# Kernel tuning notes

Hardware: AMD Instinct MI355X
Metric: run time of the kernel (lower is better)

The kernel has to match this reference:

```python
import jax, jax.numpy as jnp
from jax import lax
import numpy as np

HIDDEN = 40
NUM_LAYERS = 7
B, H, W = 16, 64, 64
KS = 7
PAD = KS // 2  # 3

# mask for conv_2d type 'A': zero rows below center, zero right-of-center in
# the center row, and zero the center tap itself
_m = np.ones((1, 1, KS, KS), np.float32)
_m[:, :, PAD + 1:, :] = 0
_m[:, :, PAD, PAD + 1:] = 0
_m[:, :, PAD, PAD] = 0
MASK_A = jnp.asarray(_m)


def conv2d(x, w, pad):
    return lax.conv_general_dilated(x, w, (1, 1), pad,
                                    dimension_numbers=('NCHW', 'OIHW', 'NCHW'))


def setup_inputs() -> dict:
    key = jax.random.key(0)
    ks = jax.random.split(key, 12)
    s = 0.05
    return {
        'input_tensor': jax.random.normal(ks[0], (B, 1, H, W), jnp.float32),
        'target_tensor': jax.random.normal(ks[1], (B, 1, H, W), jnp.float32),
        # masked conv_2d(7,1,80) applied to target
        'w_is': jax.random.normal(ks[2], (2 * HIDDEN, 1, KS, KS), jnp.float32) * s,
        'b_is': jnp.ones((2 * HIDDEN,), jnp.float32),
        # conv_i_s: Conv2d(1, 80, 7, pad 3)
        'w_cis': jax.random.normal(ks[3], (2 * HIDDEN, 1, KS, KS), jnp.float32) * s,
        'b_cis': jax.random.normal(ks[4], (2 * HIDDEN,), jnp.float32) * s,
        # row convs: Conv2d(40, 40, [1,3], pad [0,1])
        'w_rh': jax.random.normal(ks[5], (HIDDEN, HIDDEN, 1, 3), jnp.float32) * s,
        'b_rh': jax.random.normal(ks[6], (HIDDEN,), jnp.float32) * s,
        'w_rc': jax.random.normal(ks[7], (HIDDEN, HIDDEN, 1, 3), jnp.float32) * s,
        'b_rc': jax.random.normal(ks[8], (HIDDEN,), jnp.float32) * s,
        # per-layer cell 1x1 convs: 40 -> 160, stacked over layers
        'w_cell': jax.random.normal(ks[9], (NUM_LAYERS, 4 * HIDDEN, HIDDEN), jnp.float32) * s,
        'b_cell': jax.random.normal(ks[10], (NUM_LAYERS, 4 * HIDDEN), jnp.float32) * s,
        # conv_out: Conv2d(40, 256, 1)
        'w_out': jax.random.normal(ks[11], (256, HIDDEN), jnp.float32) * s,
        'b_out': jnp.zeros((256,), jnp.float32),
    }


def reference(input_tensor, target_tensor, w_is, b_is, w_cis, b_cis,
              w_rh, b_rh, w_rc, b_rc, w_cell, b_cell, w_out, b_out):
    same7 = ((PAD, PAD), (PAD, PAD))
    # i_s = cat([conv_i_s(input), masked_conv(target)], dim=1) -> [B, 160, H, W]
    i_s_input = conv2d(input_tensor, w_cis, same7) + b_cis[None, :, None, None]
    i_s_target = conv2d(target_tensor, w_is * MASK_A, same7) + b_is[None, :, None, None]
    i_s = jnp.concatenate([i_s_input, i_s_target], axis=1)

    h0 = jnp.zeros((B, HIDDEN, 1, W), i_s.dtype)
    c0 = jnp.zeros((B, HIDDEN, 1, W), i_s.dtype)

    def step(carry, x_t):  # x_t: [B, 160, 1, W]
        h, c = carry
        h = conv2d(h, w_rh, ((0, 0), (1, 1))) + b_rh[None, :, None, None]
        c = conv2d(c, w_rc, ((0, 0), (1, 1))) + b_rc[None, :, None, None]
        for l in range(NUM_LAYERS):
            h_conv = jnp.einsum('oc,bcrw->borw', w_cell[l], h) + b_cell[l][None, :, None, None]
            combined = x_t + h_conv
            cc_i, cc_f, cc_o, cc_g = jnp.split(combined, 4, axis=1)
            i = jax.nn.sigmoid(cc_i)
            f = jax.nn.sigmoid(cc_f)
            o = jax.nn.sigmoid(cc_o)
            g = jnp.tanh(cc_g)
            c = f * c + i * g
            h = o * jnp.tanh(c)
        return (h, c), h

    xs = jnp.moveaxis(i_s, 2, 0)[:, :, :, None, :]  # [H, B, 160, 1, W]
    _, hs = lax.scan(step, (h0, c0), xs)            # hs: [H, B, 40, 1, W]
    hidden = jnp.moveaxis(hs[:, :, :, 0, :], 0, 2)  # [B, 40, H, W]
    out = jnp.einsum('oc,bchw->bohw', w_out, hidden) + b_out[None, :, None, None]
    return jax.nn.relu(out)
```

## Files before the change

kernel.cpp:

```cpp
#include <hip/hip_runtime.h>


typedef __bf16 bf16x8 __attribute__((ext_vector_type(8)));
typedef __bf16 bf16x4 __attribute__((ext_vector_type(4)));
typedef float  f32x4  __attribute__((ext_vector_type(4)));

#define SC1 (-1.44269504089f)
#define SC2 (-2.88539008178f)

#define STP 56
#define HLS 896
#define CWS 17

#define BARRIER_LGKM() __asm__ volatile("s_waitcnt lgkmcnt(0)\ns_barrier" ::: "memory")

__global__ __launch_bounds__(256) void prep_kernel(
        const float* __restrict__ wcell, const float* __restrict__ wrh,
        const float* __restrict__ wrc, const float* __restrict__ bcell,
        const float* __restrict__ brh, const float* __restrict__ brc,
        __bf16* __restrict__ wsA) {
    int i = blockIdx.x * 256 + threadIdx.x;
    if (i >= 120832) return;
    float val = 0.0f;
    if (i < 35840) {
        int j = i & 7, lane = (i >> 3) & 63, lm = i >> 9;
        int mt = lm % 10, l = lm / 10;
        int k = (lane >> 4) * 8 + j, m = lane & 15, r = m & 3;
        int row = r * 40 + 4 * mt + (m >> 2);
        val = wcell[(l * 160 + row) * 40 + k] * (r == 3 ? SC2 : SC1);
    } else if (i < 71680) {
        int i2 = i - 35840;
        int j = i2 & 7, lane = (i2 >> 3) & 63, lm = i2 >> 9;
        int mt = lm % 10, l = lm / 10;
        int k = 32 + (lane >> 4) * 8 + j, m = lane & 15, r = m & 3;
        int row = r * 40 + 4 * mt + (m >> 2);
        float s = (r == 3 ? SC2 : SC1);
        if (k < 40)       val = wcell[(l * 160 + row) * 40 + k] * s;
        else if (k == 40) val = bcell[l * 160 + row] * s;
    } else if (i < 80896) {
        int i3 = i - 71680;
        int j = i3 & 7, lane = (i3 >> 3) & 63, idx = i3 >> 9;
        int mtc = idx % 3, t2 = idx / 3, dx = t2 % 3, cv = t2 / 3;
        int k = (lane >> 4) * 8 + j;
        int ch = 16 * mtc + (lane & 15);
        const float* w = cv ? wrc : wrh;
        if (ch < 40) val = w[(ch * 40 + k) * 3 + dx];
    } else if (i < 90112) {
        int i4 = i - 80896;
        int j = i4 & 7, lane = (i4 >> 3) & 63, idx = i4 >> 9;
        int mtc = idx % 3, t2 = idx / 3, dx = t2 % 3, cv = t2 / 3;
        int k = 32 + (lane >> 4) * 8 + j;
        int ch = 16 * mtc + (lane & 15);
        if (ch < 40) {
            const float* w = cv ? wrc : wrh;
            if (k < 40)                    val = w[(ch * 40 + k) * 3 + dx];
            else if (k == 40 && dx == 1)   val = (cv ? brc : brh)[ch];
        }
    } else if (i < 105472) {
        int i5 = i - 90112;
        int j = i5 & 7, lane = (i5 >> 3) & 63, idx = i5 >> 9;
        int mt = idx % 10, dx = idx / 10;
        int k = (lane >> 4) * 8 + j, m = lane & 15, r = m & 3;
        int row = r * 40 + 4 * mt + (m >> 2);
        float s = (r == 3 ? SC2 : SC1);
        float acc = 0.0f;
        for (int mm = 0; mm < 40; mm++)
            acc = __builtin_fmaf(wcell[row * 40 + mm],
                                 wrh[(mm * 40 + k) * 3 + dx], acc);
        val = acc * s;
    } else {
        int i6 = i - 105472;
        int j = i6 & 7, lane = (i6 >> 3) & 63, idx = i6 >> 9;
        int mt = idx % 10, dx = idx / 10;
        int k = 32 + (lane >> 4) * 8 + j, m = lane & 15, r = m & 3;
        int row = r * 40 + 4 * mt + (m >> 2);
        float s = (r == 3 ? SC2 : SC1);
        if (k < 40) {
            float acc = 0.0f;
            for (int mm = 0; mm < 40; mm++)
                acc = __builtin_fmaf(wcell[row * 40 + mm],
                                     wrh[(mm * 40 + k) * 3 + dx], acc);
            val = acc * s;
        } else if (k == 40 && dx == 1) {
            float acc = bcell[row];
            for (int mm = 0; mm < 40; mm++)
                acc = __builtin_fmaf(wcell[row * 40 + mm], brh[mm], acc);
            val = acc * s;
        }
    }
    wsA[i] = (__bf16)val;
}

__global__ __launch_bounds__(256) void conv7_kernel(
        const float* __restrict__ inp, const float* __restrict__ tgt,
        const float* __restrict__ w_is, const float* __restrict__ b_is,
        const float* __restrict__ w_cis, const float* __restrict__ b_cis,
        float* __restrict__ x_ws) {
    int b = blockIdx.x >> 6, y = blockIdx.x & 63;
    int tid = threadIdx.x, qq = tid >> 6, w = tid & 63;
    const float* ib = inp + b * 4096;
    const float* tb = tgt + b * 4096;
    float pin[7][7], ptg[4][7];
#pragma unroll
    for (int dy = 0; dy < 7; dy++) {
        int yy = y + dy - 3;
#pragma unroll
        for (int dx = 0; dx < 7; dx++) {
            int xx = w + dx - 3;
            bool ok = (yy >= 0 && yy < 64 && xx >= 0 && xx < 64);
            pin[dy][dx] = ok ? ib[yy * 64 + xx] : 0.0f;
            if (dy < 4) ptg[dy][dx] = ok ? tb[yy * 64 + xx] : 0.0f;
        }
    }
    int g = w >> 4, l16 = w & 15;
    for (int j = 0; j < 10; j++) {
        int cc = 4 * j + qq;
        int ccu = __builtin_amdgcn_readfirstlane(cc);
        float a0 = b_cis[ccu], a1 = b_cis[40 + ccu];
        float a2 = b_is[ccu], a3 = b_is[40 + ccu];
        const float* w0 = w_cis + ccu * 49;
        const float* w1 = w_cis + (40 + ccu) * 49;
        const float* w2 = w_is + ccu * 49;
        const float* w3 = w_is + (40 + ccu) * 49;
#pragma unroll
        for (int dy = 0; dy < 7; dy++)
#pragma unroll
            for (int dx = 0; dx < 7; dx++) {
                a0 = __builtin_fmaf(w0[dy * 7 + dx], pin[dy][dx], a0);
                a1 = __builtin_fmaf(w1[dy * 7 + dx], pin[dy][dx], a1);
            }
#pragma unroll
        for (int dy = 0; dy < 3; dy++)
#pragma unroll
            for (int dx = 0; dx < 7; dx++) {
                a2 = __builtin_fmaf(w2[dy * 7 + dx], ptg[dy][dx], a2);
                a3 = __builtin_fmaf(w3[dy * 7 + dx], ptg[dy][dx], a3);
            }
#pragma unroll
        for (int dx = 0; dx < 3; dx++) {
            a2 = __builtin_fmaf(w2[21 + dx], ptg[3][dx], a2);
            a3 = __builtin_fmaf(w3[21 + dx], ptg[3][dx], a3);
        }
        size_t idx = (size_t)((((b * 64 + y) * 4 + g) * 10 + j) * 4 + qq) * 64
                     + l16 * 4;
        *(f32x4*)&x_ws[idx] = f32x4{a0 * SC1, a1 * SC1, a2 * SC1, a3 * SC2};
    }
}

__global__ __launch_bounds__(640, 1) void rnn_kernel(
        const float* __restrict__ x_ws, const __bf16* __restrict__ wsA,
        float* __restrict__ hid_ws,
        unsigned long long* __restrict__ halo_ws) {
    __shared__ __align__(16) __bf16 hC[18 * STP + 64];
    __shared__ __align__(16) __bf16 cC[18 * STP + 64];
    __shared__ __align__(16) __bf16 hL[2 * HLS + 32];
    __shared__ float cwf[40 * CWS];
    __shared__ unsigned cflag[4];

    const int bid = blockIdx.x, g = bid >> 4, b = bid & 15;
    const int tid = threadIdx.x, wv = tid >> 6, lane = tid & 63;
    const int q = lane >> 4, l16 = lane & 15, cc = 4 * wv + q;
    const int W0 = g * 16;

    for (int i = tid; i < 536; i += 640) {
        ((float*)hC)[i] = 0.0f;
        ((float*)cC)[i] = 0.0f;
    }
    for (int i = tid; i < 912; i += 640)
        ((float*)hL)[i] = 0.0f;
    for (int i = tid; i < 40 * CWS; i += 640) cwf[i] = 0.0f;
    if (tid < 4) cflag[tid] = 0xFFFFFFFFu;
    __syncthreads();
    if (tid < 18) { hC[tid * STP + 40] = (__bf16)1.0f; cC[tid * STP + 40] = (__bf16)1.0f; }
    if (tid < 32) hL[(tid >> 4) * HLS + (tid & 15) * STP + 40] = (__bf16)1.0f;
    __syncthreads();

    bf16x8 a0c[6], a1c[6];
#pragma unroll
    for (int l = 1; l < 7; l++) {
        a0c[l - 1] = *(const bf16x8*)&wsA[((l * 10 + wv) * 64 + lane) * 8];
        a1c[l - 1] = *(const bf16x8*)&wsA[35840 + ((l * 10 + wv) * 64 + lane) * 8];
    }
    bf16x8 f0c[3], f1c[3];
#pragma unroll
    for (int dx = 0; dx < 3; dx++) {
        f0c[dx] = *(const bf16x8*)&wsA[90112 + ((dx * 10 + wv) * 64 + lane) * 8];
        f1c[dx] = *(const bf16x8*)&wsA[105472 + ((dx * 10 + wv) * 64 + lane) * 8];
    }
    bf16x8 cva0[3], cva1[3];
    if (wv >= 3 && wv < 6) {
        int mtc = wv - 3;
#pragma unroll
        for (int dx = 0; dx < 3; dx++) {
            int it = (3 + dx) * 3 + mtc;
            cva0[dx] = *(const bf16x8*)&wsA[71680 + (it * 64 + lane) * 8];
            cva1[dx] = *(const bf16x8*)&wsA[80896 + (it * 64 + lane) * 8];
        }
    }

    float c_reg = 0.0f;
    const size_t xstride = 10240;
    const size_t xbase0 = (size_t)(b * 64) * xstride
        + (((size_t)g * 10 + wv) * 4 + q) * 64 + l16 * 4;
    f32x4 xv = *(const f32x4*)&x_ws[xbase0];

    for (int t = 0; t < 64; t++) {
        f32x4 xn = xv;
        if (t < 63) xn = *(const f32x4*)&x_ws[xbase0 + (size_t)(t + 1) * xstride];

        if (wv >= 3 && wv < 6) {
            f32x4 ac = f32x4{0.f, 0.f, 0.f, 0.f};
#pragma unroll
            for (int dx = 0; dx < 3; dx++) {
                bf16x8 b0 = *(const bf16x8*)&cC[(l16 + dx) * STP + q * 8];
                bf16x8 b1 = *(const bf16x8*)&cC[(l16 + dx) * STP + 32 + q * 8];
                ac = __builtin_amdgcn_mfma_f32_16x16x32_bf16(cva0[dx], b0, ac, 0, 0, 0);
                ac = __builtin_amdgcn_mfma_f32_16x16x32_bf16(cva1[dx], b1, ac, 0, 0, 0);
            }
            int mtc = wv - 3, ch0 = 16 * mtc + 4 * q;
            if (ch0 < 40) {
#pragma unroll
                for (int r = 0; r < 4; r++) cwf[(ch0 + r) * CWS + l16] = ac[r];
            }
            __asm__ volatile("s_waitcnt lgkmcnt(0)" ::: "memory");
            if (lane == 0)
                __hip_atomic_store(&cflag[mtc], (unsigned)t,
                                   __ATOMIC_RELAXED, __HIP_MEMORY_SCOPE_WORKGROUP);
        }

        f32x4 acc0 = f32x4{0.f, 0.f, 0.f, 0.f};
#pragma unroll
        for (int dx = 0; dx < 3; dx++) {
            bf16x8 b0 = *(const bf16x8*)&hC[(l16 + dx) * STP + q * 8];
            bf16x8 b1 = *(const bf16x8*)&hC[(l16 + dx) * STP + 32 + q * 8];
            acc0 = __builtin_amdgcn_mfma_f32_16x16x32_bf16(f0c[dx], b0, acc0, 0, 0, 0);
            acc0 = __builtin_amdgcn_mfma_f32_16x16x32_bf16(f1c[dx], b1, acc0, 0, 0, 0);
        }
        {
            int jj = wv >> 2;
            while (__hip_atomic_load(&cflag[jj], __ATOMIC_RELAXED,
                                     __HIP_MEMORY_SCOPE_WORKGROUP) != (unsigned)t)
                __builtin_amdgcn_s_sleep(1);
            __asm__ volatile("" ::: "memory");
        }

#pragma unroll
        for (int l = 0; l < 7; l++) {
            f32x4 acc;
            if (l == 0) {
                acc = acc0;
                c_reg = cwf[cc * CWS + l16];
            } else {
                const __bf16* hb = &hL[(l & 1) * HLS];
                bf16x8 b0 = *(const bf16x8*)&hb[l16 * STP + q * 8];
                bf16x8 b1 = *(const bf16x8*)&hb[l16 * STP + 32 + q * 8];
                acc = __builtin_amdgcn_mfma_f32_16x16x32_bf16(
                    a0c[l - 1], b0, f32x4{0.f, 0.f, 0.f, 0.f}, 0, 0, 0);
                acc = __builtin_amdgcn_mfma_f32_16x16x32_bf16(a1c[l - 1], b1, acc, 0, 0, 0);
            }
            float Ei = __builtin_amdgcn_exp2f(fminf(acc[0] + xv[0], 44.f));
            float Ef = __builtin_amdgcn_exp2f(fminf(acc[1] + xv[1], 44.f));
            float Eo = __builtin_amdgcn_exp2f(fminf(acc[2] + xv[2], 44.f));
            float Eg = __builtin_amdgcn_exp2f(fminf(acc[3] + xv[3], 44.f));
            float f = __builtin_amdgcn_rcpf(1.0f + Ef);
            float ig = (1.0f - Eg) * __builtin_amdgcn_rcpf((1.0f + Ei) * (1.0f + Eg));
            float c = __builtin_fmaf(f, c_reg, ig);
            c_reg = c;
            float Ec = __builtin_amdgcn_exp2f(fminf(SC2 * c, 44.f));
            float h = (1.0f - Ec) * __builtin_amdgcn_rcpf((1.0f + Eo) * (1.0f + Ec));
            if (l < 6) {
                hL[((l + 1) & 1) * HLS + l16 * STP + cc] = (__bf16)h;
                BARRIER_LGKM();
            } else {
                hC[(l16 + 1) * STP + cc] = (__bf16)h;
                cC[(l16 + 1) * STP + cc] = (__bf16)c;
                hid_ws[(size_t)((b * 64 + t) * 40 + cc) * 64 + W0 + l16] = h;
                if (t < 63) {
                    unsigned short h16 = __builtin_bit_cast(unsigned short, (__bf16)h);
                    unsigned short c16 = __builtin_bit_cast(unsigned short, (__bf16)c);
                    unsigned long long v = ((unsigned long long)(unsigned)t << 32)
                        | ((unsigned)c16 << 16) | (unsigned)h16;
                    if (l16 == 0 && g > 0)
                        __hip_atomic_store(
                            &halo_ws[((bid * 2 + 0) * 2 + (t & 1)) * 40 + cc], v,
                            __ATOMIC_RELAXED, __HIP_MEMORY_SCOPE_AGENT);
                    if (l16 == 15 && g < 3)
                        __hip_atomic_store(
                            &halo_ws[((bid * 2 + 1) * 2 + (t & 1)) * 40 + cc], v,
                            __ATOMIC_RELAXED, __HIP_MEMORY_SCOPE_AGENT);
                }
            }
        }

        if (t < 63) {
            if (wv == 8 && g > 0 && lane < 40) {
                const unsigned long long* src =
                    &halo_ws[(((bid - 16) * 2 + 1) * 2 + (t & 1)) * 40 + lane];
                unsigned long long v = __hip_atomic_load(
                    src, __ATOMIC_RELAXED, __HIP_MEMORY_SCOPE_AGENT);
                while ((unsigned)(v >> 32) != (unsigned)t) {
                    __builtin_amdgcn_s_sleep(1);
                    v = __hip_atomic_load(src, __ATOMIC_RELAXED,
                                          __HIP_MEMORY_SCOPE_AGENT);
                }
                hC[lane] = __builtin_bit_cast(__bf16, (unsigned short)(v & 0xffffu));
                cC[lane] = __builtin_bit_cast(__bf16, (unsigned short)((v >> 16) & 0xffffu));
            }
            if (wv == 9 && g < 3 && lane < 40) {
                const unsigned long long* src =
                    &halo_ws[(((bid + 16) * 2 + 0) * 2 + (t & 1)) * 40 + lane];
                unsigned long long v = __hip_atomic_load(
                    src, __ATOMIC_RELAXED, __HIP_MEMORY_SCOPE_AGENT);
                while ((unsigned)(v >> 32) != (unsigned)t) {
                    __builtin_amdgcn_s_sleep(1);
                    v = __hip_atomic_load(src, __ATOMIC_RELAXED,
                                          __HIP_MEMORY_SCOPE_AGENT);
                }
                hC[17 * STP + lane] = __builtin_bit_cast(__bf16, (unsigned short)(v & 0xffffu));
                cC[17 * STP + lane] = __builtin_bit_cast(__bf16, (unsigned short)((v >> 16) & 0xffffu));
            }
        }
        BARRIER_LGKM();
        xv = xn;
    }
}

__global__ __launch_bounds__(256) void out_kernel(
        const float* __restrict__ hid_ws, const float* __restrict__ w_out,
        const float* __restrict__ b_out, float* __restrict__ out) {
    __shared__ float wlds[40 * 264];
    __shared__ float hlds[40 * 64];
    int b = blockIdx.x >> 6, y = blockIdx.x & 63;
    int tid = threadIdx.x;
    for (int i = tid; i < 10240; i += 256) {
        int o = i / 40, k = i - o * 40;
        wlds[k * 264 + o] = w_out[i];
    }
    const float* hbp = hid_ws + (size_t)(b * 64 + y) * 40 * 64;
    for (int i = tid; i < 2560; i += 256) hlds[i] = hbp[i];
    __syncthreads();

    int tn = tid & 7, tm = tid >> 3;
    int wbase = tn * 8, obase = tm * 8;
    float acc[8][8];
#pragma unroll
    for (int io = 0; io < 8; io++)
#pragma unroll
        for (int iw = 0; iw < 8; iw++) acc[io][iw] = 0.0f;

    for (int k = 0; k < 40; k++) {
        f32x4 hA = *(const f32x4*)&hlds[k * 64 + wbase];
        f32x4 hB = *(const f32x4*)&hlds[k * 64 + wbase + 4];
        f32x4 wA = *(const f32x4*)&wlds[k * 264 + obase];
        f32x4 wB = *(const f32x4*)&wlds[k * 264 + obase + 4];
#pragma unroll
        for (int io = 0; io < 8; io++) {
            float wo = (io < 4) ? wA[io] : wB[io - 4];
#pragma unroll
            for (int iw = 0; iw < 8; iw++) {
                float hx = (iw < 4) ? hA[iw] : hB[iw - 4];
                acc[io][iw] = __builtin_fmaf(wo, hx, acc[io][iw]);
            }
        }
    }
#pragma unroll
    for (int io = 0; io < 8; io++) {
        int o = obase + io;
        float bo = b_out[o];
        f32x4 s0, s1;
#pragma unroll
        for (int iw = 0; iw < 4; iw++)
            s0[iw] = fmaxf(acc[io][iw] + bo, 0.0f);
#pragma unroll
        for (int iw = 0; iw < 4; iw++)
            s1[iw] = fmaxf(acc[io][iw + 4] + bo, 0.0f);
        float* ob = out + (size_t)((b * 256 + o) * 64 + y) * 64 + wbase;
        *(f32x4*)ob = s0;
        *(f32x4*)(ob + 4) = s1;
    }
}

extern "C" void kernel_launch(void* const* d_in, const int* in_sizes, int n_in,
                              void* d_out, int out_size, void* d_ws,
                              size_t ws_size, hipStream_t stream) {
    const float* input  = (const float*)d_in[0];
    const float* target = (const float*)d_in[1];
    const float* w_is   = (const float*)d_in[2];
    const float* b_is   = (const float*)d_in[3];
    const float* w_cis  = (const float*)d_in[4];
    const float* b_cis  = (const float*)d_in[5];
    const float* w_rh   = (const float*)d_in[6];
    const float* b_rh   = (const float*)d_in[7];
    const float* w_rc   = (const float*)d_in[8];
    const float* b_rc   = (const float*)d_in[9];
    const float* w_cell = (const float*)d_in[10];
    const float* b_cell = (const float*)d_in[11];
    const float* w_out  = (const float*)d_in[12];
    const float* b_out  = (const float*)d_in[13];
    float* out = (float*)d_out;

    char* ws = (char*)d_ws;
    float*              x_ws    = (float*)ws;
    float*              hid_ws  = (float*)(ws + 41943040);
    __bf16*             wsA     = (__bf16*)(ws + 52428800);
    unsigned long long* halo_ws = (unsigned long long*)(ws + 52670464);

    prep_kernel<<<472, 256, 0, stream>>>(w_cell, w_rh, w_rc, b_cell, b_rh,
                                         b_rc, wsA);
    conv7_kernel<<<1024, 256, 0, stream>>>(input, target, w_is, b_is, w_cis,
                                           b_cis, x_ws);
    rnn_kernel<<<64, 640, 0, stream>>>(x_ws, wsA, hid_ws, halo_ws);
    out_kernel<<<1024, 256, 0, stream>>>(hid_ws, w_out, b_out, out);
}
```

Baseline: 369.4 us.

## Give each RNN wave two gate tiles and shrink the block to eight waves

The recurrent kernel moves from 10 waves, each owning one 16-row gate tile, to 5 compute waves that each own two tiles, plus 3 waves that handle the c-conv and halo exchange. The B operand loaded from LDS is shared by both tiles, so fewer waves take part in each of the per-layer barriers and fewer LDS reads are issued. In exchange, each compute wave runs a longer serial chain on the critical path and holds twice as many weight registers, which raises register pressure.

Result: slower. 395.8 us (+7.1%).

```diff
diff --git a/kernel.cpp b/kernel.cpp
--- a/kernel.cpp
+++ b/kernel.cpp
@@ -147,7 +147,7 @@
     }
 }
 
-__global__ __launch_bounds__(640, 1) void rnn_kernel(
+__global__ __launch_bounds__(512, 1) void rnn_kernel(
         const float* __restrict__ x_ws, const __bf16* __restrict__ wsA,
         float* __restrict__ hid_ws,
         unsigned long long* __restrict__ halo_ws) {
@@ -159,37 +159,46 @@
 
     const int bid = blockIdx.x, g = bid >> 4, b = bid & 15;
     const int tid = threadIdx.x, wv = tid >> 6, lane = tid & 63;
-    const int q = lane >> 4, l16 = lane & 15, cc = 4 * wv + q;
+    const int q = lane >> 4, l16 = lane & 15;
+    const int cc0 = 8 * wv + q;
     const int W0 = g * 16;
 
-    for (int i = tid; i < 536; i += 640) {
+    for (int i = tid; i < 536; i += 512) {
         ((float*)hC)[i] = 0.0f;
         ((float*)cC)[i] = 0.0f;
     }
-    for (int i = tid; i < 912; i += 640)
+    for (int i = tid; i < 912; i += 512)
         ((float*)hL)[i] = 0.0f;
-    for (int i = tid; i < 40 * CWS; i += 640) cwf[i] = 0.0f;
+    for (int i = tid; i < 40 * CWS; i += 512) cwf[i] = 0.0f;
     if (tid < 4) cflag[tid] = 0xFFFFFFFFu;
     __syncthreads();
     if (tid < 18) { hC[tid * STP + 40] = (__bf16)1.0f; cC[tid * STP + 40] = (__bf16)1.0f; }
     if (tid < 32) hL[(tid >> 4) * HLS + (tid & 15) * STP + 40] = (__bf16)1.0f;
     __syncthreads();
 
-    bf16x8 a0c[6], a1c[6];
-#pragma unroll
-    for (int l = 1; l < 7; l++) {
-        a0c[l - 1] = *(const bf16x8*)&wsA[((l * 10 + wv) * 64 + lane) * 8];
-        a1c[l - 1] = *(const bf16x8*)&wsA[35840 + ((l * 10 + wv) * 64 + lane) * 8];
-    }
-    bf16x8 f0c[3], f1c[3];
-#pragma unroll
-    for (int dx = 0; dx < 3; dx++) {
-        f0c[dx] = *(const bf16x8*)&wsA[90112 + ((dx * 10 + wv) * 64 + lane) * 8];
-        f1c[dx] = *(const bf16x8*)&wsA[105472 + ((dx * 10 + wv) * 64 + lane) * 8];
+    bf16x8 a0c[6][2], a1c[6][2];
+    bf16x8 f0c[3][2], f1c[3][2];
+    if (wv < 5) {
+#pragma unroll
+        for (int l = 1; l < 7; l++)
+#pragma unroll
+            for (int tt = 0; tt < 2; tt++) {
+                int mt = 2 * wv + tt;
+                a0c[l - 1][tt] = *(const bf16x8*)&wsA[((l * 10 + mt) * 64 + lane) * 8];
+                a1c[l - 1][tt] = *(const bf16x8*)&wsA[35840 + ((l * 10 + mt) * 64 + lane) * 8];
+            }
+#pragma unroll
+        for (int dx = 0; dx < 3; dx++)
+#pragma unroll
+            for (int tt = 0; tt < 2; tt++) {
+                int mt = 2 * wv + tt;
+                f0c[dx][tt] = *(const bf16x8*)&wsA[90112 + ((dx * 10 + mt) * 64 + lane) * 8];
+                f1c[dx][tt] = *(const bf16x8*)&wsA[105472 + ((dx * 10 + mt) * 64 + lane) * 8];
+            }
     }
     bf16x8 cva0[3], cva1[3];
-    if (wv >= 3 && wv < 6) {
-        int mtc = wv - 3;
+    if (wv >= 5) {
+        int mtc = wv - 5;
 #pragma unroll
         for (int dx = 0; dx < 3; dx++) {
             int it = (3 + dx) * 3 + mtc;
@@ -198,17 +207,25 @@
         }
     }
 
-    float c_reg = 0.0f;
     const size_t xstride = 10240;
-    const size_t xbase0 = (size_t)(b * 64) * xstride
-        + (((size_t)g * 10 + wv) * 4 + q) * 64 + l16 * 4;
-    f32x4 xv = *(const f32x4*)&x_ws[xbase0];
+    size_t xb[2];
+    {
+        int mt0 = (wv < 5) ? 2 * wv : 0, mt1 = (wv < 5) ? 2 * wv + 1 : 0;
+        xb[0] = (size_t)(b * 64) * xstride + (((size_t)g * 10 + mt0) * 4 + q) * 64 + l16 * 4;
+        xb[1] = (size_t)(b * 64) * xstride + (((size_t)g * 10 + mt1) * 4 + q) * 64 + l16 * 4;
+    }
+    f32x4 xv[2], xn[2];
+    xv[0] = *(const f32x4*)&x_ws[xb[0]];
+    xv[1] = *(const f32x4*)&x_ws[xb[1]];
 
     for (int t = 0; t < 64; t++) {
-        f32x4 xn = xv;
-        if (t < 63) xn = *(const f32x4*)&x_ws[xbase0 + (size_t)(t + 1) * xstride];
-
-        if (wv >= 3 && wv < 6) {
+        xn[0] = xv[0]; xn[1] = xv[1];
+        if (wv < 5 && t < 63) {
+            xn[0] = *(const f32x4*)&x_ws[xb[0] + (size_t)(t + 1) * xstride];
+            xn[1] = *(const f32x4*)&x_ws[xb[1] + (size_t)(t + 1) * xstride];
+        }
+
+        if (wv >= 5) {
             f32x4 ac = f32x4{0.f, 0.f, 0.f, 0.f};
 #pragma unroll
             for (int dx = 0; dx < 3; dx++) {
@@ -217,7 +234,7 @@
                 ac = __builtin_amdgcn_mfma_f32_16x16x32_bf16(cva0[dx], b0, ac, 0, 0, 0);
                 ac = __builtin_amdgcn_mfma_f32_16x16x32_bf16(cva1[dx], b1, ac, 0, 0, 0);
             }
-            int mtc = wv - 3, ch0 = 16 * mtc + 4 * q;
+            int mtc = wv - 5, ch0 = 16 * mtc + 4 * q;
             if (ch0 < 40) {
 #pragma unroll
                 for (int r = 0; r < 4; r++) cwf[(ch0 + r) * CWS + l16] = ac[r];
@@ -228,72 +245,89 @@
                                    __ATOMIC_RELAXED, __HIP_MEMORY_SCOPE_WORKGROUP);
         }
 
-        f32x4 acc0 = f32x4{0.f, 0.f, 0.f, 0.f};
-#pragma unroll
-        for (int dx = 0; dx < 3; dx++) {
-            bf16x8 b0 = *(const bf16x8*)&hC[(l16 + dx) * STP + q * 8];
-            bf16x8 b1 = *(const bf16x8*)&hC[(l16 + dx) * STP + 32 + q * 8];
-            acc0 = __builtin_amdgcn_mfma_f32_16x16x32_bf16(f0c[dx], b0, acc0, 0, 0, 0);
-            acc0 = __builtin_amdgcn_mfma_f32_16x16x32_bf16(f1c[dx], b1, acc0, 0, 0, 0);
-        }
-        {
-            int jj = wv >> 2;
+        f32x4 acc0[2];
+        if (wv < 5) {
+            acc0[0] = f32x4{0.f, 0.f, 0.f, 0.f};
+            acc0[1] = f32x4{0.f, 0.f, 0.f, 0.f};
+#pragma unroll
+            for (int dx = 0; dx < 3; dx++) {
+                bf16x8 b0 = *(const bf16x8*)&hC[(l16 + dx) * STP + q * 8];
+                bf16x8 b1 = *(const bf16x8*)&hC[(l16 + dx) * STP + 32 + q * 8];
+#pragma unroll
+                for (int tt = 0; tt < 2; tt++) {
+                    acc0[tt] = __builtin_amdgcn_mfma_f32_16x16x32_bf16(f0c[dx][tt], b0, acc0[tt], 0, 0, 0);
+                    acc0[tt] = __builtin_amdgcn_mfma_f32_16x16x32_bf16(f1c[dx][tt], b1, acc0[tt], 0, 0, 0);
+                }
+            }
+            int jj = wv >> 1;
             while (__hip_atomic_load(&cflag[jj], __ATOMIC_RELAXED,
                                      __HIP_MEMORY_SCOPE_WORKGROUP) != (unsigned)t)
                 __builtin_amdgcn_s_sleep(1);
             __asm__ volatile("" ::: "memory");
         }
 
+        float crg[2];
 #pragma unroll
         for (int l = 0; l < 7; l++) {
-            f32x4 acc;
-            if (l == 0) {
-                acc = acc0;
-                c_reg = cwf[cc * CWS + l16];
-            } else {
-                const __bf16* hb = &hL[(l & 1) * HLS];
-                bf16x8 b0 = *(const bf16x8*)&hb[l16 * STP + q * 8];
-                bf16x8 b1 = *(const bf16x8*)&hb[l16 * STP + 32 + q * 8];
-                acc = __builtin_amdgcn_mfma_f32_16x16x32_bf16(
-                    a0c[l - 1], b0, f32x4{0.f, 0.f, 0.f, 0.f}, 0, 0, 0);
-                acc = __builtin_amdgcn_mfma_f32_16x16x32_bf16(a1c[l - 1], b1, acc, 0, 0, 0);
-            }
-            float Ei = __builtin_amdgcn_exp2f(fminf(acc[0] + xv[0], 44.f));
-            float Ef = __builtin_amdgcn_exp2f(fminf(acc[1] + xv[1], 44.f));
-            float Eo = __builtin_amdgcn_exp2f(fminf(acc[2] + xv[2], 44.f));
-            float Eg = __builtin_amdgcn_exp2f(fminf(acc[3] + xv[3], 44.f));
-            float f = __builtin_amdgcn_rcpf(1.0f + Ef);
-            float ig = (1.0f - Eg) * __builtin_amdgcn_rcpf((1.0f + Ei) * (1.0f + Eg));
-            float c = __builtin_fmaf(f, c_reg, ig);
-            c_reg = c;
-            float Ec = __builtin_amdgcn_exp2f(fminf(SC2 * c, 44.f));
-            float h = (1.0f - Ec) * __builtin_amdgcn_rcpf((1.0f + Eo) * (1.0f + Ec));
-            if (l < 6) {
-                hL[((l + 1) & 1) * HLS + l16 * STP + cc] = (__bf16)h;
-                BARRIER_LGKM();
-            } else {
-                hC[(l16 + 1) * STP + cc] = (__bf16)h;
-                cC[(l16 + 1) * STP + cc] = (__bf16)c;
-                hid_ws[(size_t)((b * 64 + t) * 40 + cc) * 64 + W0 + l16] = h;
-                if (t < 63) {
-                    unsigned short h16 = __builtin_bit_cast(unsigned short, (__bf16)h);
-                    unsigned short c16 = __builtin_bit_cast(unsigned short, (__bf16)c);
-                    unsigned long long v = ((unsigned long long)(unsigned)t << 32)
-                        | ((unsigned)c16 << 16) | (unsigned)h16;
-                    if (l16 == 0 && g > 0)
-                        __hip_atomic_store(
-                            &halo_ws[((bid * 2 + 0) * 2 + (t & 1)) * 40 + cc], v,
-                            __ATOMIC_RELAXED, __HIP_MEMORY_SCOPE_AGENT);
-                    if (l16 == 15 && g < 3)
-                        __hip_atomic_store(
-                            &halo_ws[((bid * 2 + 1) * 2 + (t & 1)) * 40 + cc], v,
-                            __ATOMIC_RELAXED, __HIP_MEMORY_SCOPE_AGENT);
+            if (wv < 5) {
+                f32x4 av[2];
+                if (l == 0) {
+                    av[0] = acc0[0]; av[1] = acc0[1];
+                    crg[0] = cwf[cc0 * CWS + l16];
+                    crg[1] = cwf[(cc0 + 4) * CWS + l16];
+                } else {
+                    const __bf16* hb = &hL[(l & 1) * HLS];
+                    bf16x8 b0 = *(const bf16x8*)&hb[l16 * STP + q * 8];
+                    bf16x8 b1 = *(const bf16x8*)&hb[l16 * STP + 32 + q * 8];
+#pragma unroll
+                    for (int tt = 0; tt < 2; tt++) {
+                        av[tt] = __builtin_amdgcn_mfma_f32_16x16x32_bf16(
+                            a0c[l - 1][tt], b0, f32x4{0.f, 0.f, 0.f, 0.f}, 0, 0, 0);
+                        av[tt] = __builtin_amdgcn_mfma_f32_16x16x32_bf16(
+                            a1c[l - 1][tt], b1, av[tt], 0, 0, 0);
+                    }
                 }
-            }
+#pragma unroll
+                for (int tt = 0; tt < 2; tt++) {
+                    int cc = cc0 + 4 * tt;
+                    float Ei = __builtin_amdgcn_exp2f(fminf(av[tt][0] + xv[tt][0], 44.f));
+                    float Ef = __builtin_amdgcn_exp2f(fminf(av[tt][1] + xv[tt][1], 44.f));
+                    float Eo = __builtin_amdgcn_exp2f(fminf(av[tt][2] + xv[tt][2], 44.f));
+                    float Eg = __builtin_amdgcn_exp2f(fminf(av[tt][3] + xv[tt][3], 44.f));
+                    float f = __builtin_amdgcn_rcpf(1.0f + Ef);
+                    float ig = (1.0f - Eg) * __builtin_amdgcn_rcpf((1.0f + Ei) * (1.0f + Eg));
+                    float c = __builtin_fmaf(f, crg[tt], ig);
+                    crg[tt] = c;
+                    float Ec = __builtin_amdgcn_exp2f(fminf(SC2 * c, 44.f));
+                    float h = (1.0f - Ec) * __builtin_amdgcn_rcpf((1.0f + Eo) * (1.0f + Ec));
+                    if (l < 6) {
+                        hL[((l + 1) & 1) * HLS + l16 * STP + cc] = (__bf16)h;
+                    } else {
+                        hC[(l16 + 1) * STP + cc] = (__bf16)h;
+                        cC[(l16 + 1) * STP + cc] = (__bf16)c;
+                        hid_ws[(size_t)((b * 64 + t) * 40 + cc) * 64 + W0 + l16] = h;
+                        if (t < 63) {
+                            unsigned short h16 = __builtin_bit_cast(unsigned short, (__bf16)h);
+                            unsigned short c16 = __builtin_bit_cast(unsigned short, (__bf16)c);
+                            unsigned long long v = ((unsigned long long)(unsigned)t << 32)
+                                | ((unsigned)c16 << 16) | (unsigned)h16;
+                            if (l16 == 0 && g > 0)
+                                __hip_atomic_store(
+                                    &halo_ws[((bid * 2 + 0) * 2 + (t & 1)) * 40 + cc], v,
+                                    __ATOMIC_RELAXED, __HIP_MEMORY_SCOPE_AGENT);
+                            if (l16 == 15 && g < 3)
+                                __hip_atomic_store(
+                                    &halo_ws[((bid * 2 + 1) * 2 + (t & 1)) * 40 + cc], v,
+                                    __ATOMIC_RELAXED, __HIP_MEMORY_SCOPE_AGENT);
+                        }
+                    }
+                }
+            }
+            if (l < 6) BARRIER_LGKM();
         }
 
         if (t < 63) {
-            if (wv == 8 && g > 0 && lane < 40) {
+            if (wv == 5 && g > 0 && lane < 40) {
                 const unsigned long long* src =
                     &halo_ws[(((bid - 16) * 2 + 1) * 2 + (t & 1)) * 40 + lane];
                 unsigned long long v = __hip_atomic_load(
@@ -306,7 +340,7 @@
                 hC[lane] = __builtin_bit_cast(__bf16, (unsigned short)(v & 0xffffu));
                 cC[lane] = __builtin_bit_cast(__bf16, (unsigned short)((v >> 16) & 0xffffu));
             }
-            if (wv == 9 && g < 3 && lane < 40) {
+            if (wv == 6 && g < 3 && lane < 40) {
                 const unsigned long long* src =
                     &halo_ws[(((bid + 16) * 2 + 0) * 2 + (t & 1)) * 40 + lane];
                 unsigned long long v = __hip_atomic_load(
@@ -321,7 +355,7 @@
             }
         }
         BARRIER_LGKM();
-        xv = xn;
+        xv[0] = xn[0]; xv[1] = xn[1];
     }
 }
 
@@ -409,6 +443,6 @@
                                          b_rc, wsA);
     conv7_kernel<<<1024, 256, 0, stream>>>(input, target, w_is, b_is, w_cis,
                                            b_cis, x_ws);
-    rnn_kernel<<<64, 640, 0, stream>>>(x_ws, wsA, hid_ws, halo_ws);
+    rnn_kernel<<<64, 512, 0, stream>>>(x_ws, wsA, hid_ws, halo_ws);
     out_kernel<<<1024, 256, 0, stream>>>(hid_ws, w_out, b_out, out);
 }
```

## Fuse conv7 into RNN kernel with worker blocks and an atomic completion counter

Applied to the files above, without the earlier changes.

Merges the 7x7 input convolution and the recurrent kernel into one launch. 176 extra worker blocks compute x_ws and bump a global atomic counter, while the 64 RNN blocks load their weights and spin on that counter before starting the scan. This saves one kernel launch and lets the RNN setup overlap the convolution. The cost is that all 240 blocks must be co-resident for the spin-wait to be safe, and the wait loop has a timeout that could let the RNN read incomplete data.

After: 458.4 us. 1.24x slower.

```diff
diff --git a/kernel.cpp b/kernel.cpp
--- a/kernel.cpp
+++ b/kernel.cpp
@@ -11,6 +11,7 @@
 #define STP 56
 #define HLS 896
 #define CWS 17
+#define NWRK 176u
 
 #define BARRIER_LGKM() __asm__ volatile("s_waitcnt lgkmcnt(0)\ns_barrier" ::: "memory")
 
@@ -18,9 +19,12 @@
         const float* __restrict__ wcell, const float* __restrict__ wrh,
         const float* __restrict__ wrc, const float* __restrict__ bcell,
         const float* __restrict__ brh, const float* __restrict__ brc,
-        __bf16* __restrict__ wsA) {
+        __bf16* __restrict__ wsA, unsigned* __restrict__ xcnt) {
     int i = blockIdx.x * 256 + threadIdx.x;
-    if (i >= 120832) return;
+    if (i >= 120832) {
+        if (i == 120832) xcnt[0] = 0u;
+        return;
+    }
     float val = 0.0f;
     if (i < 35840) {
         int j = i & 7, lane = (i >> 3) & 63, lm = i >> 9;
@@ -91,74 +95,86 @@
     wsA[i] = (__bf16)val;
 }
 
-__global__ __launch_bounds__(256) void conv7_kernel(
+__global__ __launch_bounds__(640, 1) void fused_kernel(
         const float* __restrict__ inp, const float* __restrict__ tgt,
         const float* __restrict__ w_is, const float* __restrict__ b_is,
         const float* __restrict__ w_cis, const float* __restrict__ b_cis,
-        float* __restrict__ x_ws) {
-    int b = blockIdx.x >> 6, y = blockIdx.x & 63;
-    int tid = threadIdx.x, qq = tid >> 6, w = tid & 63;
-    const float* ib = inp + b * 4096;
-    const float* tb = tgt + b * 4096;
-    float pin[7][7], ptg[4][7];
-#pragma unroll
-    for (int dy = 0; dy < 7; dy++) {
-        int yy = y + dy - 3;
-#pragma unroll
-        for (int dx = 0; dx < 7; dx++) {
-            int xx = w + dx - 3;
-            bool ok = (yy >= 0 && yy < 64 && xx >= 0 && xx < 64);
-            pin[dy][dx] = ok ? ib[yy * 64 + xx] : 0.0f;
-            if (dy < 4) ptg[dy][dx] = ok ? tb[yy * 64 + xx] : 0.0f;
-        }
-    }
-    int g = w >> 4, l16 = w & 15;
-    for (int j = 0; j < 10; j++) {
-        int cc = 4 * j + qq;
-        int ccu = __builtin_amdgcn_readfirstlane(cc);
-        float a0 = b_cis[ccu], a1 = b_cis[40 + ccu];
-        float a2 = b_is[ccu], a3 = b_is[40 + ccu];
-        const float* w0 = w_cis + ccu * 49;
-        const float* w1 = w_cis + (40 + ccu) * 49;
-        const float* w2 = w_is + ccu * 49;
-        const float* w3 = w_is + (40 + ccu) * 49;
-#pragma unroll
-        for (int dy = 0; dy < 7; dy++)
-#pragma unroll
-            for (int dx = 0; dx < 7; dx++) {
-                a0 = __builtin_fmaf(w0[dy * 7 + dx], pin[dy][dx], a0);
-                a1 = __builtin_fmaf(w1[dy * 7 + dx], pin[dy][dx], a1);
-            }
-#pragma unroll
-        for (int dy = 0; dy < 3; dy++)
-#pragma unroll
-            for (int dx = 0; dx < 7; dx++) {
-                a2 = __builtin_fmaf(w2[dy * 7 + dx], ptg[dy][dx], a2);
-                a3 = __builtin_fmaf(w3[dy * 7 + dx], ptg[dy][dx], a3);
-            }
-#pragma unroll
-        for (int dx = 0; dx < 3; dx++) {
-            a2 = __builtin_fmaf(w2[21 + dx], ptg[3][dx], a2);
-            a3 = __builtin_fmaf(w3[21 + dx], ptg[3][dx], a3);
-        }
-        size_t idx = (size_t)((((b * 64 + y) * 4 + g) * 10 + j) * 4 + qq) * 64
-                     + l16 * 4;
-        *(f32x4*)&x_ws[idx] = f32x4{a0 * SC1, a1 * SC1, a2 * SC1, a3 * SC2};
-    }
-}
-
-__global__ __launch_bounds__(640, 1) void rnn_kernel(
-        const float* __restrict__ x_ws, const __bf16* __restrict__ wsA,
-        float* __restrict__ hid_ws,
-        unsigned long long* __restrict__ halo_ws) {
-    __shared__ __align__(16) __bf16 hC[18 * STP + 64];
-    __shared__ __align__(16) __bf16 cC[18 * STP + 64];
-    __shared__ __align__(16) __bf16 hL[2 * HLS + 32];
-    __shared__ float cwf[40 * CWS];
+        float* __restrict__ x_ws, const __bf16* __restrict__ wsA,
+        float* __restrict__ hid_ws, unsigned long long* __restrict__ halo_ws,
+        unsigned* __restrict__ xcnt) {
+    __shared__ __align__(16) unsigned char smem[83968];
     __shared__ unsigned cflag[4];
-
-    const int bid = blockIdx.x, g = bid >> 4, b = bid & 15;
-    const int tid = threadIdx.x, wv = tid >> 6, lane = tid & 63;
+    const int bid = blockIdx.x;
+    const int tid = threadIdx.x;
+
+    if (bid >= 64) {
+        for (int p = bid - 64; p < 1024; p += 176) {
+            const int y = p >> 4, b = p & 15;
+            const int j = tid >> 6, w = tid & 63;
+            const float* ib = inp + b * 4096;
+            const float* tb = tgt + b * 4096;
+            float pin[7][7], ptg[4][7];
+#pragma unroll
+            for (int dy = 0; dy < 7; dy++) {
+                int yy = y + dy - 3;
+#pragma unroll
+                for (int dx = 0; dx < 7; dx++) {
+                    int xx = w + dx - 3;
+                    bool ok = (yy >= 0 && yy < 64 && xx >= 0 && xx < 64);
+                    pin[dy][dx] = ok ? ib[yy * 64 + xx] : 0.0f;
+                    if (dy < 4) ptg[dy][dx] = ok ? tb[yy * 64 + xx] : 0.0f;
+                }
+            }
+            int g = w >> 4, l16 = w & 15;
+#pragma unroll 1
+            for (int qq = 0; qq < 4; qq++) {
+                int cc = 4 * j + qq;
+                int ccu = __builtin_amdgcn_readfirstlane(cc);
+                float a0 = b_cis[ccu], a1 = b_cis[40 + ccu];
+                float a2 = b_is[ccu], a3 = b_is[40 + ccu];
+                const float* w0 = w_cis + ccu * 49;
+                const float* w1 = w_cis + (40 + ccu) * 49;
+                const float* w2 = w_is + ccu * 49;
+                const float* w3 = w_is + (40 + ccu) * 49;
+#pragma unroll
+                for (int dy = 0; dy < 7; dy++)
+#pragma unroll
+                    for (int dx = 0; dx < 7; dx++) {
+                        a0 = __builtin_fmaf(w0[dy * 7 + dx], pin[dy][dx], a0);
+                        a1 = __builtin_fmaf(w1[dy * 7 + dx], pin[dy][dx], a1);
+                    }
+#pragma unroll
+                for (int dy = 0; dy < 3; dy++)
+#pragma unroll
+                    for (int dx = 0; dx < 7; dx++) {
+                        a2 = __builtin_fmaf(w2[dy * 7 + dx], ptg[dy][dx], a2);
+                        a3 = __builtin_fmaf(w3[dy * 7 + dx], ptg[dy][dx], a3);
+                    }
+#pragma unroll
+                for (int dx = 0; dx < 3; dx++) {
+                    a2 = __builtin_fmaf(w2[21 + dx], ptg[3][dx], a2);
+                    a3 = __builtin_fmaf(w3[21 + dx], ptg[3][dx], a3);
+                }
+                size_t idx = (size_t)((((b * 64 + y) * 4 + g) * 10 + j) * 4 + qq) * 64
+                             + l16 * 4;
+                *(f32x4*)&x_ws[idx] = f32x4{a0 * SC1, a1 * SC1, a2 * SC1, a3 * SC2};
+            }
+        }
+        __threadfence();
+        __syncthreads();
+        if (tid == 0)
+            __hip_atomic_fetch_add(xcnt, 1u, __ATOMIC_RELEASE,
+                                   __HIP_MEMORY_SCOPE_AGENT);
+        return;
+    }
+
+    __bf16* hC  = (__bf16*)smem;
+    __bf16* cC  = (__bf16*)(smem + 4096);
+    __bf16* hL  = (__bf16*)(smem + 8192);
+    float*  cwf = (float*)(smem + 16384);
+
+    const int g = bid >> 4, b = bid & 15;
+    const int wv = tid >> 6, lane = tid & 63;
     const int q = lane >> 4, l16 = lane & 15, cc = 4 * wv + q;
     const int W0 = g * 16;
 
@@ -197,6 +213,16 @@
             cva1[dx] = *(const bf16x8*)&wsA[80896 + (it * 64 + lane) * 8];
         }
     }
+
+    if (tid == 0) {
+        int gk = 0;
+        while (__hip_atomic_load(xcnt, __ATOMIC_ACQUIRE,
+                                 __HIP_MEMORY_SCOPE_AGENT) < NWRK) {
+            if (++gk > (1 << 17)) break;
+            __builtin_amdgcn_s_sleep(8);
+        }
+    }
+    __syncthreads();
 
     float c_reg = 0.0f;
     const size_t xstride = 10240;
@@ -404,11 +430,12 @@
     float*              hid_ws  = (float*)(ws + 41943040);
     __bf16*             wsA     = (__bf16*)(ws + 52428800);
     unsigned long long* halo_ws = (unsigned long long*)(ws + 52670464);
-
-    prep_kernel<<<472, 256, 0, stream>>>(w_cell, w_rh, w_rc, b_cell, b_rh,
-                                         b_rc, wsA);
-    conv7_kernel<<<1024, 256, 0, stream>>>(input, target, w_is, b_is, w_cis,
-                                           b_cis, x_ws);
-    rnn_kernel<<<64, 640, 0, stream>>>(x_ws, wsA, hid_ws, halo_ws);
+    unsigned*           xcnt    = (unsigned*)(ws + 52752384);
+
+    prep_kernel<<<473, 256, 0, stream>>>(w_cell, w_rh, w_rc, b_cell, b_rh,
+                                         b_rc, wsA, xcnt);
+    fused_kernel<<<240, 640, 0, stream>>>(input, target, w_is, b_is, w_cis,
+                                          b_cis, x_ws, wsA, hid_ws, halo_ws,
+                                          xcnt);
     out_kernel<<<1024, 256, 0, stream>>>(hid_ws, w_out, b_out, out);
 }
```

## Fuse output 1x1 conv and ReLU into RNN kernel via bf16 MFMA

Applied to the files above, without the earlier changes.

Removes the separate out_kernel and the hidden-state workspace round trip. The RNN kernel now computes the 256-channel output projection for the previous row from the bf16 h tile in LDS using MFMA, with the bias folded in as an extra K element. Waves 0-7 do this work inside the serial timestep loop, and the last row is handled after the loop. This saves one launch and the global write and read of hidden, but adds MFMA work and many scattered global stores to the latency-critical recurrence, and the projection now uses bf16 instead of fp32.

New measurement: 366.6 us (median of 2 runs). About the same (-0.8%).

```diff
diff --git a/kernel.cpp b/kernel.cpp
--- a/kernel.cpp
+++ b/kernel.cpp
@@ -18,9 +18,10 @@
         const float* __restrict__ wcell, const float* __restrict__ wrh,
         const float* __restrict__ wrc, const float* __restrict__ bcell,
         const float* __restrict__ brh, const float* __restrict__ brc,
+        const float* __restrict__ w_out, const float* __restrict__ b_out,
         __bf16* __restrict__ wsA) {
     int i = blockIdx.x * 256 + threadIdx.x;
-    if (i >= 120832) return;
+    if (i >= 137216) return;
     float val = 0.0f;
     if (i < 35840) {
         int j = i & 7, lane = (i >> 3) & 63, lm = i >> 9;
@@ -68,7 +69,7 @@
             acc = __builtin_fmaf(wcell[row * 40 + mm],
                                  wrh[(mm * 40 + k) * 3 + dx], acc);
         val = acc * s;
-    } else {
+    } else if (i < 120832) {
         int i6 = i - 105472;
         int j = i6 & 7, lane = (i6 >> 3) & 63, idx = i6 >> 9;
         int mt = idx % 10, dx = idx / 10;
@@ -87,6 +88,19 @@
                 acc = __builtin_fmaf(wcell[row * 40 + mm], brh[mm], acc);
             val = acc * s;
         }
+    } else if (i < 129024) {
+        int i7 = i - 120832;
+        int j = i7 & 7, lane = (i7 >> 3) & 63, ot = i7 >> 9;
+        int k = (lane >> 4) * 8 + j;
+        int o = ot * 16 + (lane & 15);
+        val = w_out[o * 40 + k];
+    } else {
+        int i8 = i - 129024;
+        int j = i8 & 7, lane = (i8 >> 3) & 63, ot = i8 >> 9;
+        int k = 32 + (lane >> 4) * 8 + j;
+        int o = ot * 16 + (lane & 15);
+        if (k < 40)       val = w_out[o * 40 + k];
+        else if (k == 40) val = b_out[o];
     }
     wsA[i] = (__bf16)val;
 }
@@ -149,8 +163,7 @@
 
 __global__ __launch_bounds__(640, 1) void rnn_kernel(
         const float* __restrict__ x_ws, const __bf16* __restrict__ wsA,
-        float* __restrict__ hid_ws,
-        unsigned long long* __restrict__ halo_ws) {
+        unsigned long long* __restrict__ halo_ws, float* __restrict__ out) {
     __shared__ __align__(16) __bf16 hC[18 * STP + 64];
     __shared__ __align__(16) __bf16 cC[18 * STP + 64];
     __shared__ __align__(16) __bf16 hL[2 * HLS + 32];
@@ -197,6 +210,15 @@
             cva1[dx] = *(const bf16x8*)&wsA[80896 + (it * 64 + lane) * 8];
         }
     }
+    bf16x8 o0c[2], o1c[2];
+    if (wv < 8) {
+#pragma unroll
+        for (int tt = 0; tt < 2; tt++) {
+            int ot = 2 * wv + tt;
+            o0c[tt] = *(const bf16x8*)&wsA[120832 + (ot * 64 + lane) * 8];
+            o1c[tt] = *(const bf16x8*)&wsA[129024 + (ot * 64 + lane) * 8];
+        }
+    }
 
     float c_reg = 0.0f;
     const size_t xstride = 10240;
@@ -236,6 +258,24 @@
             acc0 = __builtin_amdgcn_mfma_f32_16x16x32_bf16(f0c[dx], b0, acc0, 0, 0, 0);
             acc0 = __builtin_amdgcn_mfma_f32_16x16x32_bf16(f1c[dx], b1, acc0, 0, 0, 0);
         }
+
+        if (t > 0 && wv < 8) {
+            int y = t - 1;
+            bf16x8 bo0 = *(const bf16x8*)&hC[(l16 + 1) * STP + q * 8];
+            bf16x8 bo1 = *(const bf16x8*)&hC[(l16 + 1) * STP + 32 + q * 8];
+#pragma unroll
+            for (int tt = 0; tt < 2; tt++) {
+                f32x4 oa = __builtin_amdgcn_mfma_f32_16x16x32_bf16(
+                    o0c[tt], bo0, f32x4{0.f, 0.f, 0.f, 0.f}, 0, 0, 0);
+                oa = __builtin_amdgcn_mfma_f32_16x16x32_bf16(o1c[tt], bo1, oa, 0, 0, 0);
+                int o0 = (2 * wv + tt) * 16 + 4 * q;
+#pragma unroll
+                for (int r = 0; r < 4; r++)
+                    out[((size_t)(b * 256 + o0 + r) * 64 + y) * 64 + W0 + l16] =
+                        fmaxf(oa[r], 0.0f);
+            }
+        }
+
         {
             int jj = wv >> 2;
             while (__hip_atomic_load(&cflag[jj], __ATOMIC_RELAXED,
@@ -274,7 +314,6 @@
             } else {
                 hC[(l16 + 1) * STP + cc] = (__bf16)h;
                 cC[(l16 + 1) * STP + cc] = (__bf16)c;
-                hid_ws[(size_t)((b * 64 + t) * 40 + cc) * 64 + W0 + l16] = h;
                 if (t < 63) {
                     unsigned short h16 = __builtin_bit_cast(unsigned short, (__bf16)h);
                     unsigned short c16 = __builtin_bit_cast(unsigned short, (__bf16)c);
@@ -323,60 +362,21 @@
         BARRIER_LGKM();
         xv = xn;
     }
-}
-
-__global__ __launch_bounds__(256) void out_kernel(
-        const float* __restrict__ hid_ws, const float* __restrict__ w_out,
-        const float* __restrict__ b_out, float* __restrict__ out) {
-    __shared__ float wlds[40 * 264];
-    __shared__ float hlds[40 * 64];
-    int b = blockIdx.x >> 6, y = blockIdx.x & 63;
-    int tid = threadIdx.x;
-    for (int i = tid; i < 10240; i += 256) {
-        int o = i / 40, k = i - o * 40;
-        wlds[k * 264 + o] = w_out[i];
-    }
-    const float* hbp = hid_ws + (size_t)(b * 64 + y) * 40 * 64;
-    for (int i = tid; i < 2560; i += 256) hlds[i] = hbp[i];
-    __syncthreads();
-
-    int tn = tid & 7, tm = tid >> 3;
-    int wbase = tn * 8, obase = tm * 8;
-    float acc[8][8];
-#pragma unroll
-    for (int io = 0; io < 8; io++)
-#pragma unroll
-        for (int iw = 0; iw < 8; iw++) acc[io][iw] = 0.0f;
-
-    for (int k = 0; k < 40; k++) {
-        f32x4 hA = *(const f32x4*)&hlds[k * 64 + wbase];
-        f32x4 hB = *(const f32x4*)&hlds[k * 64 + wbase + 4];
-        f32x4 wA = *(const f32x4*)&wlds[k * 264 + obase];
-        f32x4 wB = *(const f32x4*)&wlds[k * 264 + obase + 4];
-#pragma unroll
-        for (int io = 0; io < 8; io++) {
-            float wo = (io < 4) ? wA[io] : wB[io - 4];
-#pragma unroll
-            for (int iw = 0; iw < 8; iw++) {
-                float hx = (iw < 4) ? hA[iw] : hB[iw - 4];
-                acc[io][iw] = __builtin_fmaf(wo, hx, acc[io][iw]);
-            }
-        }
-    }
-#pragma unroll
-    for (int io = 0; io < 8; io++) {
-        int o = obase + io;
-        float bo = b_out[o];
-        f32x4 s0, s1;
-#pragma unroll
-        for (int iw = 0; iw < 4; iw++)
-            s0[iw] = fmaxf(acc[io][iw] + bo, 0.0f);
-#pragma unroll
-        for (int iw = 0; iw < 4; iw++)
-            s1[iw] = fmaxf(acc[io][iw + 4] + bo, 0.0f);
-        float* ob = out + (size_t)((b * 256 + o) * 64 + y) * 64 + wbase;
-        *(f32x4*)ob = s0;
-        *(f32x4*)(ob + 4) = s1;
+
+    if (wv < 8) {
+        bf16x8 bo0 = *(const bf16x8*)&hC[(l16 + 1) * STP + q * 8];
+        bf16x8 bo1 = *(const bf16x8*)&hC[(l16 + 1) * STP + 32 + q * 8];
+#pragma unroll
+        for (int tt = 0; tt < 2; tt++) {
+            f32x4 oa = __builtin_amdgcn_mfma_f32_16x16x32_bf16(
+                o0c[tt], bo0, f32x4{0.f, 0.f, 0.f, 0.f}, 0, 0, 0);
+            oa = __builtin_amdgcn_mfma_f32_16x16x32_bf16(o1c[tt], bo1, oa, 0, 0, 0);
+            int o0 = (2 * wv + tt) * 16 + 4 * q;
+#pragma unroll
+            for (int r = 0; r < 4; r++)
+                out[((size_t)(b * 256 + o0 + r) * 64 + 63) * 64 + W0 + l16] =
+                    fmaxf(oa[r], 0.0f);
+        }
     }
 }
 
@@ -401,14 +401,12 @@
 
     char* ws = (char*)d_ws;
     float*              x_ws    = (float*)ws;
-    float*              hid_ws  = (float*)(ws + 41943040);
-    __bf16*             wsA     = (__bf16*)(ws + 52428800);
-    unsigned long long* halo_ws = (unsigned long long*)(ws + 52670464);
-
-    prep_kernel<<<472, 256, 0, stream>>>(w_cell, w_rh, w_rc, b_cell, b_rh,
-                                         b_rc, wsA);
+    __bf16*             wsA     = (__bf16*)(ws + 41943040);
+    unsigned long long* halo_ws = (unsigned long long*)(ws + 42217472);
+
+    prep_kernel<<<536, 256, 0, stream>>>(w_cell, w_rh, w_rc, b_cell, b_rh,
+                                         b_rc, w_out, b_out, wsA);
     conv7_kernel<<<1024, 256, 0, stream>>>(input, target, w_is, b_is, w_cis,
                                            b_cis, x_ws);
-    rnn_kernel<<<64, 640, 0, stream>>>(x_ws, wsA, hid_ws, halo_ws);
-    out_kernel<<<1024, 256, 0, stream>>>(hid_ws, w_out, b_out, out);
+    rnn_kernel<<<64, 640, 0, stream>>>(x_ws, wsA, halo_ws, out);
 }
```
